# Optimization experiments

Measured on AMD Instinct MI355X. Metric: run time of the kernel, lower is better.

## Reference

```python
import jax, jax.numpy as jnp
import numpy as np

N = 100000
E = 600000
EL = 200000
HID = 16
HEADS = 4
NUM_NODE_TYPES = 8
NUM_EDGE_TYPES = 22
EDGE_DIM = 16


def setup_inputs() -> dict:
    key = jax.random.key(0)
    ks = jax.random.split(key, 32)
    s = 0.1
    d1, d2 = HID, HID * HEADS  # per-head dims of layer1 / layer2
    inp = {
        'x': jax.random.normal(ks[0], (N, HID), jnp.float32),
        'edge_index': jax.random.randint(ks[1], (2, E), 0, N),
        'node_type': jax.random.randint(ks[2], (N,), 0, NUM_NODE_TYPES),
        'edge_attr': jax.random.normal(ks[3], (E, EDGE_DIM), jnp.float32),
        'edge_type': jax.random.randint(ks[4], (E,), 0, NUM_EDGE_TYPES),
        'edge_label_index': jax.random.randint(ks[5], (2, EL), 0, N),
        # ---- layer 1 params (in=HID, heads=4, out-per-head=HID, concat) ----
        'Wx1': jax.random.normal(ks[6], (HID, HEADS * d1)) * s,
        'We1': jax.random.normal(ks[7], (EDGE_DIM, HEADS * d1)) * s,
        'nt1': jax.random.normal(ks[8], (NUM_NODE_TYPES, HID)) * s,
        'et1': jax.random.normal(ks[9], (NUM_EDGE_TYPES, HEADS * d1)) * s,
        'as1': jax.random.normal(ks[10], (HEADS, d1)) * s,
        'ad1': jax.random.normal(ks[11], (HEADS, d1)) * s,
        'ae1': jax.random.normal(ks[12], (HEADS, d1)) * s,
        'res1': jax.random.normal(ks[13], (HID, HEADS * d1)) * s,
        # ---- layer 2 params (in=4*HID, heads=4, out-per-head=4*HID, mean) ----
        'Wx2': jax.random.normal(ks[14], (HEADS * HID, HEADS * d2)) * s,
        'We2': jax.random.normal(ks[15], (EDGE_DIM, HEADS * d2)) * s,
        'nt2': jax.random.normal(ks[16], (NUM_NODE_TYPES, HEADS * HID)) * s,
        'et2': jax.random.normal(ks[17], (NUM_EDGE_TYPES, HEADS * d2)) * s,
        'as2': jax.random.normal(ks[18], (HEADS, d2)) * s,
        'ad2': jax.random.normal(ks[19], (HEADS, d2)) * s,
        'ae2': jax.random.normal(ks[20], (HEADS, d2)) * s,
        # ---- edge decoder (2*4*HID -> 4*HID -> 1) ----
        'W1': jax.random.normal(ks[21], (2 * HEADS * HID, HEADS * HID)) * s,
        'b1': jnp.zeros((HEADS * HID,), jnp.float32),
        'W2': jax.random.normal(ks[22], (HEADS * HID, 1)) * s,
        'b2': jnp.zeros((1,), jnp.float32),
    }
    return inp


def hgat_layer(x, edge_index, node_type, edge_attr, edge_type,
               Wx, We, nt_emb, et_emb, a_s, a_d, a_e, res_W,
               heads, d, concat, n):
    src, dst = edge_index[0], edge_index[1]
    # type-conditioned node projection -> [N, heads, d]
    h = ((x + nt_emb[node_type]) @ Wx).reshape(n, heads, d)
    # type-conditioned edge features -> [E, heads, d]
    e = (edge_attr @ We + et_emb[edge_type]).reshape(-1, heads, d)
    hs = h[src]  # [E, heads, d] gather
    hd = h[dst]
    sc = (jnp.einsum('ehd,hd->eh', hs, a_s)
          + jnp.einsum('ehd,hd->eh', hd, a_d)
          + jnp.einsum('ehd,hd->eh', e, a_e))
    sc = jax.nn.leaky_relu(sc, 0.2)
    # segment softmax over incoming edges of each destination node
    m = jax.ops.segment_max(sc, dst, num_segments=n)
    p = jnp.exp(sc - m[dst])
    den = jax.ops.segment_sum(p, dst, num_segments=n)
    alpha = p / (den[dst] + 1e-16)
    msg = alpha[:, :, None] * (hs + e)  # [E, heads, d]
    out = jax.ops.segment_sum(msg.reshape(-1, heads * d), dst, num_segments=n)
    out = out.reshape(n, heads, d)
    if concat:
        return out.reshape(n, heads * d) + x @ res_W
    else:
        return out.mean(axis=1) + x  # in-dim == out-dim: identity residual


def reference(x, edge_index, node_type, edge_attr, edge_type, edge_label_index,
              Wx1, We1, nt1, et1, as1, ad1, ae1, res1,
              Wx2, We2, nt2, et2, as2, ad2, ae2,
              W1, b1, W2, b2):
    n = x.shape[0]
    z = hgat_layer(x, edge_index, node_type, edge_attr, edge_type,
                   Wx1, We1, nt1, et1, as1, ad1, ae1, res1,
                   HEADS, HID, True, n)
    z = jax.nn.relu(z)
    z = hgat_layer(z, edge_index, node_type, edge_attr, edge_type,
                   Wx2, We2, nt2, et2, as2, ad2, ae2, None,
                   HEADS, HEADS * HID, False, n)
    # edge decoder: gather endpoint embeddings, 2-layer MLP
    row, col = edge_label_index[0], edge_label_index[1]
    zz = jnp.concatenate([z[row], z[col]], axis=-1)  # [EL, 2*4*HID]
    h = jax.nn.relu(zz @ W1 + b1)
    pred = (h @ W2 + b2).reshape(-1)
    return pred, z
```

## Files before the change

kernel.cpp:

```cpp
#include <hip/hip_runtime.h>
#include <stdint.h>

typedef unsigned short u16;
typedef unsigned int   u32;
typedef __attribute__((ext_vector_type(8))) short v8s;
typedef __attribute__((ext_vector_type(4))) float v4f;

#define NN  100000
#define NE  600000
#define NEL 200000

__device__ __forceinline__ float b2f(u16 u){ return __uint_as_float(((u32)u)<<16); }
__device__ __forceinline__ u16 f2b(float f){
  u32 u = __float_as_uint(f);
  u32 r = (u + 0x7FFFu + ((u>>16)&1u)) >> 16;
  return (u16)r;
}
__device__ __forceinline__ void unpack8(uint4 v, float* o){
  o[0]=__uint_as_float(v.x<<16); o[1]=__uint_as_float(v.x&0xffff0000u);
  o[2]=__uint_as_float(v.y<<16); o[3]=__uint_as_float(v.y&0xffff0000u);
  o[4]=__uint_as_float(v.z<<16); o[5]=__uint_as_float(v.z&0xffff0000u);
  o[6]=__uint_as_float(v.w<<16); o[7]=__uint_as_float(v.w&0xffff0000u);
}
__device__ __forceinline__ float ldf(const void* p, size_t i, int m){
  return m ? b2f(((const u16*)p)[i]) : ((const float*)p)[i];
}
__device__ __forceinline__ void ld16(const void* p, size_t off, int m, float* o){
  if (m){
    const uint4* q = (const uint4*)((const u16*)p + off);
    uint4 a=q[0], b=q[1]; unpack8(a,o); unpack8(b,o+8);
  } else {
    const float4* q = (const float4*)((const float*)p + off);
    float4 a=q[0],b=q[1],c=q[2],d=q[3];
    o[0]=a.x;o[1]=a.y;o[2]=a.z;o[3]=a.w; o[4]=b.x;o[5]=b.y;o[6]=b.z;o[7]=b.w;
    o[8]=c.x;o[9]=c.y;o[10]=c.z;o[11]=c.w; o[12]=d.x;o[13]=d.y;o[14]=d.z;o[15]=d.w;
  }
}
__device__ __forceinline__ void stf(void* p, size_t i, int m, float v){
  if (m) ((u16*)p)[i] = f2b(v); else ((float*)p)[i] = v;
}
__device__ __forceinline__ void atomAdd(float* p, float v){ unsafeAtomicAdd(p, v); }

__global__ void k_detect(const void* a0,const void* a3,const void* a6,const void* a7,
                         const void* a8,const void* a9,const void* a10,const void* a11,
                         const void* a12,const void* a13,const void* a14,const void* a15,
                         const void* a16,const void* a17,const void* a18,const void* a19,
                         const void* a20,const void* a21,const void* a23,
                         int* __restrict__ flags){
  const void* ptrs[19] = {a0,a3,a6,a7,a8,a9,a10,a11,a12,a13,a14,a15,a16,a17,a18,a19,a20,a21,a23};
  const int  idxs[19] = {0,3,6,7,8,9,10,11,12,13,14,15,16,17,18,19,20,21,23};
  int b = blockIdx.x;
  const u16* q = (const u16*)ptrs[b];
  u16 u = q[threadIdx.x];
  int e = (u>>7)&0xFF;
  bool good = (u==0) || (e>=110 && e<=141);
  unsigned long long m = __ballot(good);
  if (threadIdx.x==0) flags[idxs[b]] = (__popcll(m) >= 52) ? 1 : 0;
}

__global__ __launch_bounds__(256) void k_zero(float* __restrict__ buf, int n){
  int i = blockIdx.x*256 + threadIdx.x;
  if (i < n) buf[i] = 0.f;
}
__global__ __launch_bounds__(256) void k_stub(u16* __restrict__ out, int n){
  int i = blockIdx.x*256 + threadIdx.x;
  if (i < n) out[i] = 0;
}

__global__ __launch_bounds__(256) void k_pack(const void* __restrict__ Wx2,
                                              const int* __restrict__ flags,
                                              u32* __restrict__ Wxp){
  int m14 = flags[14];
  int i = blockIdx.x*256 + threadIdx.x;
  int k2=i>>8, col=i&255;
  u16 lo = f2b(ldf(Wx2,(size_t)(2*k2)*256+col,m14));
  u16 hi = f2b(ldf(Wx2,(size_t)(2*k2+1)*256+col,m14));
  Wxp[i] = ((u32)hi<<16)|lo;
}

__global__ __launch_bounds__(256) void k_hist(const int* __restrict__ ei, int* __restrict__ cnt){
  int e = blockIdx.x*256 + threadIdx.x;
  if (e < NE) atomicAdd(&cnt[ei[NE+e]], 1);
}
__global__ __launch_bounds__(256) void k_scan1(const int* __restrict__ cnt,
                                               int* __restrict__ row_ptr, int* __restrict__ bsum){
  __shared__ int sb[256];
  int i = blockIdx.x*256 + threadIdx.x, t = threadIdx.x;
  int c = (i < NN) ? cnt[i] : 0;
  sb[t] = c; __syncthreads();
  for (int off=1; off<256; off<<=1){
    int v = (t>=off) ? sb[t-off] : 0; __syncthreads();
    sb[t] += v; __syncthreads();
  }
  if (i < NN) row_ptr[i] = sb[t] - c;
  if (t == 255) bsum[blockIdx.x] = sb[255];
}
__global__ __launch_bounds__(512) void k_scan2(const int* __restrict__ bsum, int* __restrict__ boff){
  __shared__ int sb[512];
  int t = threadIdx.x;
  int nblk = (NN+255)/256;
  int c = (t < nblk) ? bsum[t] : 0;
  sb[t] = c; __syncthreads();
  for (int off=1; off<512; off<<=1){
    int v = (t>=off) ? sb[t-off] : 0; __syncthreads();
    sb[t] += v; __syncthreads();
  }
  boff[t] = sb[t] - c;
}
__global__ __launch_bounds__(256) void k_scan3(int* __restrict__ row_ptr, const int* __restrict__ boff){
  int i = blockIdx.x*256 + threadIdx.x;
  if (i < NN) row_ptr[i] += boff[blockIdx.x];
  if (i == 0) row_ptr[NN] = NE;
}
__global__ __launch_bounds__(256) void k_scatter(const int* __restrict__ ei, const int* __restrict__ etype,
                                                 const int* __restrict__ row_ptr,
                                                 int* __restrict__ cur, int* __restrict__ perm,
                                                 int* __restrict__ rank, int* __restrict__ se){
  int e = blockIdx.x*256 + threadIdx.x;
  if (e < NE){
    int d = ei[NE+e];
    int pos = row_ptr[d] + atomicAdd(&cur[d], 1);
    perm[pos] = e;
    rank[e] = pos;
    se[pos] = ei[e] | (etype[e]<<20);
  }
}

__global__ void k_fold(const void* __restrict__ We1, const void* __restrict__ ae1, const void* __restrict__ et1,
                       const void* __restrict__ We2, const void* __restrict__ ae2, const void* __restrict__ et2,
                       const int* __restrict__ flags,
                       float* We1a, float* et1a, float* We2a, float* et2a){
  int m7=flags[7], m12=flags[12], m9=flags[9], m15=flags[15], m20=flags[20], m17=flags[17];
  int t = threadIdx.x;
  if (t < 64){
    int k=t>>2, h=t&3; float s=0.f;
    for (int d=0; d<16; d++) s += ldf(We1,k*64+h*16+d,m7)*ldf(ae1,h*16+d,m12);
    We1a[t]=s;
  } else if (t < 152){
    int i=t-64; int k=i>>2, h=i&3; float s=0.f;
    for (int d=0; d<16; d++) s += ldf(et1,k*64+h*16+d,m9)*ldf(ae1,h*16+d,m12);
    et1a[i]=s;
  } else if (t < 216){
    int i=t-152; int k=i>>2, h=i&3; float s=0.f;
    for (int d=0; d<64; d++) s += ldf(We2,k*256+h*64+d,m15)*ldf(ae2,h*64+d,m20);
    We2a[i]=s;
  } else if (t < 304){
    int i=t-216; int k=i>>2, h=i&3; float s=0.f;
    for (int d=0; d<64; d++) s += ldf(et2,k*256+h*64+d,m17)*ldf(ae2,h*64+d,m20);
    et2a[i]=s;
  }
}

__global__ __launch_bounds__(256) void k1_node(
    const void* __restrict__ x, const int* __restrict__ ntype,
    const void* __restrict__ Wx1, const void* __restrict__ nt1, const void* __restrict__ res1,
    const void* __restrict__ as1, const void* __restrict__ ad1,
    const int* __restrict__ flags,
    float* __restrict__ h1, float* __restrict__ out1,
    float* __restrict__ ssrc1, float* __restrict__ sdst1){
  __shared__ float sWx[1024], sRes[1024], sA[64], sD[64], sNt[128];
  int m0=flags[0], m6=flags[6], m8=flags[8], m13=flags[13], m10=flags[10], m11=flags[11];
  for (int i=threadIdx.x;i<1024;i+=256){ sWx[i]=ldf(Wx1,i,m6); sRes[i]=ldf(res1,i,m13); }
  if (threadIdx.x<64){ sA[threadIdx.x]=ldf(as1,threadIdx.x,m10); sD[threadIdx.x]=ldf(ad1,threadIdx.x,m11); }
  if (threadIdx.x<128) sNt[threadIdx.x]=ldf(nt1,threadIdx.x,m8);
  __syncthreads();
  int n = blockIdx.x*256 + threadIdx.x;
  if (n >= NN) return;
  float xv[16]; ld16(x, (size_t)n*16, m0, xv);
  int nt = ntype[n];
  float xin[16];
  #pragma unroll
  for (int k=0;k<16;k++) xin[k] = xv[k] + sNt[nt*16+k];
  float ss[4]={0,0,0,0}, sd[4]={0,0,0,0};
  #pragma unroll
  for (int jq=0;jq<16;jq++){
    float sarr[4], rarr[4];
    #pragma unroll
    for (int m=0;m<4;m++){
      int j = jq*4+m;
      float s=0.f, r=0.f;
      #pragma unroll
      for (int k=0;k<16;k++){ s += xin[k]*sWx[k*64+j]; r += xv[k]*sRes[k*64+j]; }
      sarr[m]=s; rarr[m]=r;
      ss[j>>4] += s*sA[j];
      sd[j>>4] += s*sD[j];
    }
    ((float4*)(h1  + (size_t)n*64))[jq] = make_float4(sarr[0],sarr[1],sarr[2],sarr[3]);
    ((float4*)(out1+ (size_t)n*64))[jq] = make_float4(rarr[0],rarr[1],rarr[2],rarr[3]);
  }
  ((float4*)ssrc1)[n] = make_float4(ss[0],ss[1],ss[2],ss[3]);
  ((float4*)sdst1)[n] = make_float4(sd[0],sd[1],sd[2],sd[3]);
}

__global__ __launch_bounds__(256) void k_sed(
    const int* __restrict__ ei, const void* __restrict__ eattr, const int* __restrict__ etype,
    const float* __restrict__ Wea, const float* __restrict__ eta,
    const float* __restrict__ ssrc, const float* __restrict__ sdst,
    const int* __restrict__ rank,
    const int* __restrict__ flags,
    float* __restrict__ psort){
  __shared__ float sW[64], sE[88];
  int m3=flags[3];
  if (threadIdx.x<64) sW[threadIdx.x]=Wea[threadIdx.x];
  if (threadIdx.x<88) sE[threadIdx.x]=eta[threadIdx.x];
  __syncthreads();
  int e = blockIdx.x*256 + threadIdx.x;
  if (e >= NE) return;
  int s = ei[e], d = ei[NE+e], t = etype[e];
  float ea[16]; ld16(eattr, (size_t)e*16, m3, ea);
  float4 s4 = ((const float4*)ssrc)[s];
  float4 d4 = ((const float4*)sdst)[d];
  float sv[4] = { s4.x+d4.x, s4.y+d4.y, s4.z+d4.z, s4.w+d4.w };
  float pv[4];
  #pragma unroll
  for (int h=0; h<4; h++){
    float v = sE[t*4+h] + sv[h];
    #pragma unroll
    for (int k=0;k<16;k++) v += ea[k]*sW[k*4+h];
    v = v > 0.f ? v : 0.2f*v;
    v = fminf(v, 60.f);
    pv[h] = __expf(v);
  }
  ((float4*)psort)[rank[e]] = make_float4(pv[0],pv[1],pv[2],pv[3]);
}

__global__ __launch_bounds__(256) void k_msg1(
    const void* __restrict__ eattr, const void* __restrict__ et1, const void* __restrict__ We1,
    const float* __restrict__ h1, const float* __restrict__ psort,
    const int* __restrict__ row_ptr, const int* __restrict__ perm, const int* __restrict__ se,
    const int* __restrict__ flags,
    float* __restrict__ out1){
  __shared__ float sEt[22*64];
  __shared__ float sW1[16*64];
  __shared__ float sG[4][64];
  int m3=flags[3], m9=flags[9], m7=flags[7];
  for (int i=threadIdx.x;i<22*64;i+=256) sEt[i]=ldf(et1,i,m9);
  for (int i=threadIdx.x;i<16*64;i+=256) sW1[i]=ldf(We1,i,m7);
  __syncthreads();
  int j = threadIdx.x & 63;
  int h = j>>4, jk = j&15;
  int wid = threadIdx.x>>6;
  for (int it=0; it<8; ++it){
    int n = (blockIdx.x*4 + wid)*8 + it;
    int beg=row_ptr[n], end=row_ptr[n+1];
    float sp=0.f, acc=0.f, gacc=0.f;
    int i=beg;
    for (; i+1<end; i+=2){
      int st0=se[i], st1=se[i+1];
      float4 p0=((const float4*)psort)[i], p1=((const float4*)psort)[i+1];
      int pe0=perm[i], pe1=perm[i+1];
      int s0=st0&0xFFFFF, t0=st0>>20;
      int s1=st1&0xFFFFF, t1=st1>>20;
      float ph0 = (h==0?p0.x:h==1?p0.y:h==2?p0.z:p0.w);
      float ph1 = (h==0?p1.x:h==1?p1.y:h==2?p1.z:p1.w);
      float hv0 = h1[(size_t)s0*64+j];
      float hv1 = h1[(size_t)s1*64+j];
      float ea0 = ldf(eattr,(size_t)pe0*16+jk,m3);
      float ea1 = ldf(eattr,(size_t)pe1*16+jk,m3);
      sp   += ph0 + ph1;
      acc  += ph0*(hv0+sEt[t0*64+j]) + ph1*(hv1+sEt[t1*64+j]);
      gacc += ph0*ea0 + ph1*ea1;
    }
    if (i<end){
      int st0=se[i];
      float4 p0=((const float4*)psort)[i];
      int pe0=perm[i];
      int s0=st0&0xFFFFF, t0=st0>>20;
      float ph0 = (h==0?p0.x:h==1?p0.y:h==2?p0.z:p0.w);
      sp   += ph0;
      acc  += ph0*(h1[(size_t)s0*64+j]+sEt[t0*64+j]);
      gacc += ph0*ldf(eattr,(size_t)pe0*16+jk,m3);
    }
    float rd = 1.f/(sp+1e-16f);
    sG[wid][j] = gacc*rd;
    float proj=0.f;
    #pragma unroll
    for (int k=0;k<16;k++) proj += sG[wid][h*16+k]*sW1[k*64+j];
    out1[(size_t)n*64+j] += acc*rd + proj;
  }
}

__global__ __launch_bounds__(256) void k5_node2(
    const int* __restrict__ ntype,
    const u32* __restrict__ Wxp, const void* __restrict__ nt2,
    const void* __restrict__ as2, const void* __restrict__ ad2,
    const int* __restrict__ flags,
    const float* __restrict__ out1, float* __restrict__ zfin,
    u16* __restrict__ h2, float* __restrict__ ssrc2, float* __restrict__ sdst2){
  __shared__ u32   sWp[32*256];
  __shared__ float sNt[512];
  __shared__ float sAs[256], sAd[256];
  __shared__ float sZ[4][8][64];
  __shared__ float sR[4][2][256];
  int m16=flags[16], m18=flags[18], m19=flags[19];
  for (int i=threadIdx.x;i<32*256;i+=256) sWp[i] = Wxp[i];
  for (int i=threadIdx.x;i<512;i+=256) sNt[i]=ldf(nt2,i,m16);
  sAs[threadIdx.x]=ldf(as2,threadIdx.x,m18);
  sAd[threadIdx.x]=ldf(ad2,threadIdx.x,m19);
  __syncthreads();
  int slot=threadIdx.x>>6, j=threadIdx.x&63;
  int base=(blockIdx.x*4+slot)*8;
  #pragma unroll
  for (int i=0;i<8;i++){
    int n=base+i;
    float z = out1[(size_t)n*64+j]; z = fmaxf(z, 0.f);
    zfin[(size_t)n*64+j] = z;
    sZ[slot][i][j] = z + sNt[(ntype[n]<<6)|j];
  }
  __syncthreads();
  float acc[8][4];
  #pragma unroll
  for (int i=0;i<8;i++){ acc[i][0]=0;acc[i][1]=0;acc[i][2]=0;acc[i][3]=0; }
  for (int k2=0;k2<32;k2++){
    u32 w0p=sWp[k2*256+j], w1p=sWp[k2*256+64+j], w2p=sWp[k2*256+128+j], w3p=sWp[k2*256+192+j];
    float w0l=__uint_as_float(w0p<<16), w0h=__uint_as_float(w0p&0xffff0000u);
    float w1l=__uint_as_float(w1p<<16), w1h=__uint_as_float(w1p&0xffff0000u);
    float w2l=__uint_as_float(w2p<<16), w2h=__uint_as_float(w2p&0xffff0000u);
    float w3l=__uint_as_float(w3p<<16), w3h=__uint_as_float(w3p&0xffff0000u);
    #pragma unroll
    for (int i=0;i<8;i++){
      float2 zz = *(const float2*)&sZ[slot][i][k2*2];
      acc[i][0] += zz.x*w0l + zz.y*w0h;
      acc[i][1] += zz.x*w1l + zz.y*w1h;
      acc[i][2] += zz.x*w2l + zz.y*w2h;
      acc[i][3] += zz.x*w3l + zz.y*w3h;
    }
  }
  int g=j>>4, l=j&15;
  #pragma unroll
  for (int i=0;i<8;i++){
    int n=base+i;
    u32 lo = (u32)f2b(acc[i][0]) | ((u32)f2b(acc[i][1])<<16);
    u32 hi = (u32)f2b(acc[i][2]) | ((u32)f2b(acc[i][3])<<16);
    *(uint2*)&h2[(size_t)n*256 + j*4] = make_uint2(lo,hi);
    sR[slot][0][      j] = acc[i][0]*sAs[      j];
    sR[slot][0][ 64 + j] = acc[i][1]*sAs[ 64 + j];
    sR[slot][0][128 + j] = acc[i][2]*sAs[128 + j];
    sR[slot][0][192 + j] = acc[i][3]*sAs[192 + j];
    sR[slot][1][      j] = acc[i][0]*sAd[      j];
    sR[slot][1][ 64 + j] = acc[i][1]*sAd[ 64 + j];
    sR[slot][1][128 + j] = acc[i][2]*sAd[128 + j];
    sR[slot][1][192 + j] = acc[i][3]*sAd[192 + j];
    float4 v4 = *(const float4*)&sR[slot][0][g*64 + l*4];
    float4 w4 = *(const float4*)&sR[slot][1][g*64 + l*4];
    float vs = v4.x+v4.y+v4.z+v4.w;
    float vd = w4.x+w4.y+w4.z+w4.w;
    #pragma unroll
    for (int off=1; off<16; off<<=1){ vs += __shfl_xor(vs,off); vd += __shfl_xor(vd,off); }
    if (l==0){ ssrc2[(size_t)n*4+g]=vs; sdst2[(size_t)n*4+g]=vd; }
  }
}

__global__ __launch_bounds__(256) void k_msg2(
    const void* __restrict__ eattr, const void* __restrict__ et2,
    const u16* __restrict__ h2, const float* __restrict__ psort,
    const int* __restrict__ row_ptr, const int* __restrict__ perm, const int* __restrict__ se,
    const int* __restrict__ flags,
    float* __restrict__ zfin, float* __restrict__ gsum){
  __shared__ float4 sEt4[22*64];
  int m3=flags[3], m17=flags[17];
  for (int i=threadIdx.x;i<22*64;i+=256){
    int t=i>>6, j=i&63;
    sEt4[i] = make_float4(ldf(et2,(size_t)t*256+j,m17),      ldf(et2,(size_t)t*256+64+j,m17),
                          ldf(et2,(size_t)t*256+128+j,m17),  ldf(et2,(size_t)t*256+192+j,m17));
  }
  __syncthreads();
  int j = threadIdx.x & 63;
  int jh = j>>4, jk = j&15;
  int wid = threadIdx.x>>6;
  for (int it=0; it<8; ++it){
    int n = (blockIdx.x*4 + wid)*8 + it;
    int beg=row_ptr[n], end=row_ptr[n+1];
    float ds0=0,ds1=0,ds2=0,ds3=0;
    float pa0=0,pa1=0,pa2=0,pa3=0, gacc=0;
    int i=beg;
    for (; i+1<end; i+=2){
      int st0=se[i], st1=se[i+1];
      float4 q0=((const float4*)psort)[i], q1=((const float4*)psort)[i+1];
      int pe0=perm[i], pe1=perm[i+1];
      int s0=st0&0xFFFFF, t0=st0>>20;
      int s1=st1&0xFFFFF, t1=st1>>20;
      uint2 hA = *(const uint2*)&h2[(size_t)s0*256 + j*4];
      uint2 hB = *(const uint2*)&h2[(size_t)s1*256 + j*4];
      float ea0 = ldf(eattr,(size_t)pe0*16+jk,m3);
      float ea1 = ldf(eattr,(size_t)pe1*16+jk,m3);
      float4 eA = sEt4[t0*64+j], eB = sEt4[t1*64+j];
      ds0 += q0.x+q1.x; ds1 += q0.y+q1.y; ds2 += q0.z+q1.z; ds3 += q0.w+q1.w;
      pa0 += q0.x*(__uint_as_float(hA.x<<16)        +eA.x) + q1.x*(__uint_as_float(hB.x<<16)        +eB.x);
      pa1 += q0.y*(__uint_as_float(hA.x&0xffff0000u)+eA.y) + q1.y*(__uint_as_float(hB.x&0xffff0000u)+eB.y);
      pa2 += q0.z*(__uint_as_float(hA.y<<16)        +eA.z) + q1.z*(__uint_as_float(hB.y<<16)        +eB.z);
      pa3 += q0.w*(__uint_as_float(hA.y&0xffff0000u)+eA.w) + q1.w*(__uint_as_float(hB.y&0xffff0000u)+eB.w);
      float pj0 = (jh==0?q0.x:jh==1?q0.y:jh==2?q0.z:q0.w);
      float pj1 = (jh==0?q1.x:jh==1?q1.y:jh==2?q1.z:q1.w);
      gacc += pj0*ea0 + pj1*ea1;
    }
    if (i<end){
      int st0=se[i];
      float4 q0=((const float4*)psort)[i];
      int pe0=perm[i];
      int s0=st0&0xFFFFF, t0=st0>>20;
      uint2 hA = *(const uint2*)&h2[(size_t)s0*256 + j*4];
      float4 eA = sEt4[t0*64+j];
      ds0 += q0.x; ds1 += q0.y; ds2 += q0.z; ds3 += q0.w;
      pa0 += q0.x*(__uint_as_float(hA.x<<16)        +eA.x);
      pa1 += q0.y*(__uint_as_float(hA.x&0xffff0000u)+eA.y);
      pa2 += q0.z*(__uint_as_float(hA.y<<16)        +eA.z);
      pa3 += q0.w*(__uint_as_float(hA.y&0xffff0000u)+eA.w);
      float pj0 = (jh==0?q0.x:jh==1?q0.y:jh==2?q0.z:q0.w);
      gacc += pj0*ldf(eattr,(size_t)pe0*16+jk,m3);
    }
    float r0=1.f/(ds0+1e-16f), r1=1.f/(ds1+1e-16f), r2=1.f/(ds2+1e-16f), r3=1.f/(ds3+1e-16f);
    float acc = pa0*r0 + pa1*r1 + pa2*r2 + pa3*r3;
    float rj = (jh==0?r0:jh==1?r1:jh==2?r2:r3);
    zfin[(size_t)n*64+j] += 0.25f*acc;
    gsum[(size_t)n*64+j] = gacc*rj;
  }
}

__global__ __launch_bounds__(256) void k_finz(
    const float* __restrict__ gsum, const void* __restrict__ We2,
    const int* __restrict__ flags, float* __restrict__ zfin, void* __restrict__ out){
  __shared__ float sW[16*256];
  __shared__ float sG[4][64];
  int m15=flags[15], mo=flags[0];
  for (int i=threadIdx.x;i<16*256;i+=256) sW[i]=ldf(We2,i,m15);
  __syncthreads();
  int slot=threadIdx.x>>6, j=threadIdx.x&63;
  for (int nb=blockIdx.x; nb<NN/4; nb+=gridDim.x){
    int n = nb*4 + slot;
    sG[slot][j] = gsum[(size_t)n*64 + j];
    float acc = 0.f;
    #pragma unroll
    for (int h=0;h<4;h++){
      float s=0.f;
      #pragma unroll
      for (int k=0;k<16;k++) s += sG[slot][h*16+k]*sW[k*256 + h*64 + j];
      acc += s;
    }
    float zf = zfin[(size_t)n*64+j] + 0.25f*acc;
    zfin[(size_t)n*64+j] = zf;
    stf(out, (size_t)NEL + (size_t)n*64 + j, mo, zf);
  }
}

__global__ __launch_bounds__(256) void k_dec(
    const int* __restrict__ eli, const float* __restrict__ zfin,
    const void* __restrict__ W1, const u16* __restrict__ b1,
    const void* __restrict__ W2, const u16* __restrict__ b2,
    const int* __restrict__ flags,
    void* __restrict__ out){
  __shared__ v8s sB[4][4][64];
  __shared__ float sB1[64], sW2[64];
  int m21=flags[21], m23=flags[23], mo=flags[0];
  for (int idx=threadIdx.x; idx<1024; idx+=256){
    int kb=idx>>8, ct=(idx>>6)&3, l=idx&63;
    int col = ct*16 + (l&15);
    int kbase = kb*32 + ((l>>4)<<3);
    short v[8];
    #pragma unroll
    for (int i=0;i<8;i++) v[i] = (short)f2b(ldf(W1,(size_t)(kbase+i)*64+col,m21));
    sB[kb][ct][l] = *(v8s*)v;
  }
  if (threadIdx.x<64){ sB1[threadIdx.x]=b2f(b1[threadIdx.x]); sW2[threadIdx.x]=ldf(W2,threadIdx.x,m23); }
  __syncthreads();
  float b2v = b2f(b2[0]);
  int w = threadIdx.x>>6, lane = threadIdx.x&63;
  int l15 = lane&15, lk = lane>>4;
  int ngrp = NEL/64;
  for (int g = blockIdx.x; g < ngrp; g += gridDim.x){
    int e0 = g*64 + w*16;
    int eA = e0 + l15;
    int rn = eli[eA], cn = eli[NEL+eA];
    v8s a[4];
    #pragma unroll
    for (int kb=0;kb<4;kb++){
      int k = kb*32 + lk*8;
      const float* src = (k<64) ? (zfin + (size_t)rn*64 + k) : (zfin + (size_t)cn*64 + (k-64));
      float4 f0 = *(const float4*)(src);
      float4 f1 = *(const float4*)(src+4);
      short v[8] = {(short)f2b(f0.x),(short)f2b(f0.y),(short)f2b(f0.z),(short)f2b(f0.w),
                    (short)f2b(f1.x),(short)f2b(f1.y),(short)f2b(f1.z),(short)f2b(f1.w)};
      a[kb] = *(v8s*)v;
    }
    float part[4] = {0,0,0,0};
    #pragma unroll
    for (int ct=0; ct<4; ct++){
      v4f c = {0.f,0.f,0.f,0.f};
      #pragma unroll
      for (int kb=0;kb<4;kb++)
        c = __builtin_amdgcn_mfma_f32_16x16x32_bf16(a[kb], sB[kb][ct][lane], c, 0,0,0);
      int col = ct*16 + l15;
      float w2c = sW2[col], b1c = sB1[col];
      #pragma unroll
      for (int r=0;r<4;r++) part[r] += fmaxf(c[r]+b1c, 0.f) * w2c;
    }
    #pragma unroll
    for (int r=0;r<4;r++){
      float v = part[r];
      #pragma unroll
      for (int off=1; off<16; off<<=1) v += __shfl_xor(v, off);
      if (l15==0) stf(out, e0 + lk*4 + r, mo, v + b2v);
    }
  }
}

extern "C" void kernel_launch(void* const* d_in, const int* in_sizes, int n_in,
                              void* d_out, int out_size, void* d_ws, size_t ws_size,
                              hipStream_t stream){
  (void)in_sizes; (void)n_in;
  const void* x    =d_in[0];
  const int* ei    =(const int*)d_in[1];
  const int* ntype =(const int*)d_in[2];
  const void* eattr=d_in[3];
  const int* etype =(const int*)d_in[4];
  const int* eli   =(const int*)d_in[5];
  const void* Wx1=d_in[6];  const void* We1=d_in[7];  const void* nt1=d_in[8];
  const void* et1=d_in[9];  const void* as1=d_in[10]; const void* ad1=d_in[11];
  const void* ae1=d_in[12]; const void* res1=d_in[13];
  const void* Wx2=d_in[14]; const void* We2=d_in[15]; const void* nt2=d_in[16];
  const void* et2=d_in[17]; const void* as2=d_in[18]; const void* ad2=d_in[19];
  const void* ae2=d_in[20];
  const void* W1=d_in[21];  const u16* b1=(const u16*)d_in[22];
  const void* W2=d_in[23];  const u16* b2=(const u16*)d_in[24];

  const size_t NEED_BYTES = 30809572ULL * 4ULL;
  if (ws_size < NEED_BYTES){
    k_stub<<<(out_size+255)/256,256,0,stream>>>((u16*)d_out, out_size);
    return;
  }
  float* ws=(float*)d_ws;
  size_t o=0;
  int*   flags=(int*)(ws+o); o+=32;
  float* We1a =ws+o; o+=64;
  float* et1a =ws+o; o+=96;
  float* We2a =ws+o; o+=64;
  float* et2a =ws+o; o+=96;
  int*   cnt    =(int*)(ws+o); o+=NN;
  int*   row_ptr=(int*)(ws+o); o+=NN+4;
  int*   perm   =(int*)(ws+o); o+=NE;
  int*   bsum   =(int*)(ws+o); o+=512;
  int*   boff   =(int*)(ws+o); o+=512;
  int*   rank   =(int*)(ws+o); o+=NE;
  int*   se     =(int*)(ws+o); o+=NE;
  u32*   Wxp    =(u32*)(ws+o); o+=8192;
  float* ssrc =ws+o; o+=(size_t)NN*4;
  float* sdst =ws+o; o+=(size_t)NN*4;
  float* psort=ws+o; o+=(size_t)NE*4;
  float* slotA=ws+o; o+=(size_t)NN*64;
  float* out1 =ws+o; o+=(size_t)NN*64;
  u16*   h2   =(u16*)(ws+o); o+=(size_t)NN*128;
  float* h1   = slotA;
  float* zfin = slotA;
  float* gsum = out1;

  const int NBLK = (NN+255)/256;

  k_detect<<<19,64,0,stream>>>(x,eattr,Wx1,We1,nt1,et1,as1,ad1,ae1,res1,
                               Wx2,We2,nt2,et2,as2,ad2,ae2,W1,W2,flags);
  k_fold<<<1,320,0,stream>>>(We1,ae1,et1,We2,ae2,et2,flags,We1a,et1a,We2a,et2a);
  k_pack<<<32,256,0,stream>>>(Wx2,flags,Wxp);
  k_zero<<<(NN+255)/256,256,0,stream>>>((float*)cnt, NN);
  k_hist<<<(NE+255)/256,256,0,stream>>>(ei, cnt);
  k_scan1<<<NBLK,256,0,stream>>>(cnt, row_ptr, bsum);
  k_scan2<<<1,512,0,stream>>>(bsum, boff);
  k_scan3<<<NBLK,256,0,stream>>>(row_ptr, boff);
  k_zero<<<(NN+255)/256,256,0,stream>>>((float*)cnt, NN);
  k_scatter<<<(NE+255)/256,256,0,stream>>>(ei, etype, row_ptr, cnt, perm, rank, se);
  k1_node<<<(NN+255)/256,256,0,stream>>>(x,ntype,Wx1,nt1,res1,as1,ad1,flags,h1,out1,ssrc,sdst);
  k_sed<<<(NE+255)/256,256,0,stream>>>(ei,eattr,etype,We1a,et1a,ssrc,sdst,rank,flags,psort);
  k_msg1<<<NN/32,256,0,stream>>>(eattr,et1,We1,h1,psort,row_ptr,perm,se,flags,out1);
  k5_node2<<<NN/32,256,0,stream>>>(ntype,Wxp,nt2,as2,ad2,flags,out1,zfin,h2,ssrc,sdst);
  k_sed<<<(NE+255)/256,256,0,stream>>>(ei,eattr,etype,We2a,et2a,ssrc,sdst,rank,flags,psort);
  k_msg2<<<NN/32,256,0,stream>>>(eattr,et2,h2,psort,row_ptr,perm,se,flags,zfin,gsum);
  k_finz<<<2048,256,0,stream>>>(gsum,We2,flags,zfin,d_out);
  k_dec<<<1024,256,0,stream>>>(eli,zfin,W1,b1,W2,b2,flags,d_out);
}
```

Measured before the change: 618.9 us.

## Fuse edge attention score computation into message aggregation kernels

Removes the separate k_sed kernels that computed per-edge exp-scores into a sorted psort buffer, and drops the rank array. Each message kernel now recomputes the score inline from the edge attributes it already loads, using a 16-lane shuffle reduction against the folded edge weights plus gathered ssrc/sdst values. This saves two full edge passes, including the scattered psort writes and the later psort reads. In exchange the inner loop gains shuffles, exp and extra ssrc gathers, and layer 2 needs cross-head broadcasts.

```diff
diff --git a/kernel.cpp b/kernel.cpp
--- a/kernel.cpp
+++ b/kernel.cpp
@@ -115,13 +115,12 @@
 __global__ __launch_bounds__(256) void k_scatter(const int* __restrict__ ei, const int* __restrict__ etype,
                                                  const int* __restrict__ row_ptr,
                                                  int* __restrict__ cur, int* __restrict__ perm,
-                                                 int* __restrict__ rank, int* __restrict__ se){
+                                                 int* __restrict__ se){
   int e = blockIdx.x*256 + threadIdx.x;
   if (e < NE){
     int d = ei[NE+e];
     int pos = row_ptr[d] + atomicAdd(&cur[d], 1);
     perm[pos] = e;
-    rank[e] = pos;
     se[pos] = ei[e] | (etype[e]<<20);
   }
 }
@@ -192,84 +191,72 @@
   ((float4*)sdst1)[n] = make_float4(sd[0],sd[1],sd[2],sd[3]);
 }
 
-__global__ __launch_bounds__(256) void k_sed(
-    const int* __restrict__ ei, const void* __restrict__ eattr, const int* __restrict__ etype,
-    const float* __restrict__ Wea, const float* __restrict__ eta,
-    const float* __restrict__ ssrc, const float* __restrict__ sdst,
-    const int* __restrict__ rank,
-    const int* __restrict__ flags,
-    float* __restrict__ psort){
-  __shared__ float sW[64], sE[88];
-  int m3=flags[3];
-  if (threadIdx.x<64) sW[threadIdx.x]=Wea[threadIdx.x];
-  if (threadIdx.x<88) sE[threadIdx.x]=eta[threadIdx.x];
-  __syncthreads();
-  int e = blockIdx.x*256 + threadIdx.x;
-  if (e >= NE) return;
-  int s = ei[e], d = ei[NE+e], t = etype[e];
-  float ea[16]; ld16(eattr, (size_t)e*16, m3, ea);
-  float4 s4 = ((const float4*)ssrc)[s];
-  float4 d4 = ((const float4*)sdst)[d];
-  float sv[4] = { s4.x+d4.x, s4.y+d4.y, s4.z+d4.z, s4.w+d4.w };
-  float pv[4];
-  #pragma unroll
-  for (int h=0; h<4; h++){
-    float v = sE[t*4+h] + sv[h];
-    #pragma unroll
-    for (int k=0;k<16;k++) v += ea[k]*sW[k*4+h];
-    v = v > 0.f ? v : 0.2f*v;
-    v = fminf(v, 60.f);
-    pv[h] = __expf(v);
-  }
-  ((float4*)psort)[rank[e]] = make_float4(pv[0],pv[1],pv[2],pv[3]);
-}
-
 __global__ __launch_bounds__(256) void k_msg1(
     const void* __restrict__ eattr, const void* __restrict__ et1, const void* __restrict__ We1,
-    const float* __restrict__ h1, const float* __restrict__ psort,
+    const float* __restrict__ We1a, const float* __restrict__ et1a,
+    const float* __restrict__ ssrc, const float* __restrict__ sdst,
+    const float* __restrict__ h1,
     const int* __restrict__ row_ptr, const int* __restrict__ perm, const int* __restrict__ se,
     const int* __restrict__ flags,
     float* __restrict__ out1){
   __shared__ float sEt[22*64];
   __shared__ float sW1[16*64];
+  __shared__ float sWa[64], sEa[88];
   __shared__ float sG[4][64];
   int m3=flags[3], m9=flags[9], m7=flags[7];
   for (int i=threadIdx.x;i<22*64;i+=256) sEt[i]=ldf(et1,i,m9);
   for (int i=threadIdx.x;i<16*64;i+=256) sW1[i]=ldf(We1,i,m7);
+  if (threadIdx.x<64) sWa[threadIdx.x]=We1a[threadIdx.x];
+  if (threadIdx.x<88) sEa[threadIdx.x]=et1a[threadIdx.x];
   __syncthreads();
   int j = threadIdx.x & 63;
   int h = j>>4, jk = j&15;
   int wid = threadIdx.x>>6;
+  float wA = sWa[jk*4+h];
   for (int it=0; it<8; ++it){
     int n = (blockIdx.x*4 + wid)*8 + it;
+    float sdn = sdst[(size_t)n*4+h];
     int beg=row_ptr[n], end=row_ptr[n+1];
     float sp=0.f, acc=0.f, gacc=0.f;
     int i=beg;
     for (; i+1<end; i+=2){
       int st0=se[i], st1=se[i+1];
-      float4 p0=((const float4*)psort)[i], p1=((const float4*)psort)[i+1];
       int pe0=perm[i], pe1=perm[i+1];
       int s0=st0&0xFFFFF, t0=st0>>20;
       int s1=st1&0xFFFFF, t1=st1>>20;
-      float ph0 = (h==0?p0.x:h==1?p0.y:h==2?p0.z:p0.w);
-      float ph1 = (h==0?p1.x:h==1?p1.y:h==2?p1.z:p1.w);
+      float ea0 = ldf(eattr,(size_t)pe0*16+jk,m3);
+      float ea1 = ldf(eattr,(size_t)pe1*16+jk,m3);
       float hv0 = h1[(size_t)s0*64+j];
       float hv1 = h1[(size_t)s1*64+j];
+      float ss0 = ssrc[(size_t)s0*4+h];
+      float ss1 = ssrc[(size_t)s1*4+h];
+      float sc0 = ea0*wA, sc1 = ea1*wA;
+      sc0 += __shfl_xor(sc0,1); sc1 += __shfl_xor(sc1,1);
+      sc0 += __shfl_xor(sc0,2); sc1 += __shfl_xor(sc1,2);
+      sc0 += __shfl_xor(sc0,4); sc1 += __shfl_xor(sc1,4);
+      sc0 += __shfl_xor(sc0,8); sc1 += __shfl_xor(sc1,8);
+      float v0 = sEa[t0*4+h] + ss0 + sdn + sc0;
+      float v1 = sEa[t1*4+h] + ss1 + sdn + sc1;
+      v0 = v0>0.f ? v0 : 0.2f*v0;  v0 = fminf(v0,60.f);  float p0 = __expf(v0);
+      v1 = v1>0.f ? v1 : 0.2f*v1;  v1 = fminf(v1,60.f);  float p1 = __expf(v1);
+      sp   += p0 + p1;
+      acc  += p0*(hv0+sEt[t0*64+j]) + p1*(hv1+sEt[t1*64+j]);
+      gacc += p0*ea0 + p1*ea1;
+    }
+    if (i<end){
+      int st0=se[i]; int pe0=perm[i];
+      int s0=st0&0xFFFFF, t0=st0>>20;
       float ea0 = ldf(eattr,(size_t)pe0*16+jk,m3);
-      float ea1 = ldf(eattr,(size_t)pe1*16+jk,m3);
-      sp   += ph0 + ph1;
-      acc  += ph0*(hv0+sEt[t0*64+j]) + ph1*(hv1+sEt[t1*64+j]);
-      gacc += ph0*ea0 + ph1*ea1;
-    }
-    if (i<end){
-      int st0=se[i];
-      float4 p0=((const float4*)psort)[i];
-      int pe0=perm[i];
-      int s0=st0&0xFFFFF, t0=st0>>20;
-      float ph0 = (h==0?p0.x:h==1?p0.y:h==2?p0.z:p0.w);
-      sp   += ph0;
-      acc  += ph0*(h1[(size_t)s0*64+j]+sEt[t0*64+j]);
-      gacc += ph0*ldf(eattr,(size_t)pe0*16+jk,m3);
+      float hv0 = h1[(size_t)s0*64+j];
+      float ss0 = ssrc[(size_t)s0*4+h];
+      float sc0 = ea0*wA;
+      sc0 += __shfl_xor(sc0,1); sc0 += __shfl_xor(sc0,2);
+      sc0 += __shfl_xor(sc0,4); sc0 += __shfl_xor(sc0,8);
+      float v0 = sEa[t0*4+h] + ss0 + sdn + sc0;
+      v0 = v0>0.f ? v0 : 0.2f*v0;  v0 = fminf(v0,60.f);  float p0 = __expf(v0);
+      sp   += p0;
+      acc  += p0*(hv0+sEt[t0*64+j]);
+      gacc += p0*ea0;
     }
     float rd = 1.f/(sp+1e-16f);
     sG[wid][j] = gacc*rd;
@@ -353,61 +340,83 @@
 
 __global__ __launch_bounds__(256) void k_msg2(
     const void* __restrict__ eattr, const void* __restrict__ et2,
-    const u16* __restrict__ h2, const float* __restrict__ psort,
+    const float* __restrict__ We2a, const float* __restrict__ et2a,
+    const float* __restrict__ ssrc, const float* __restrict__ sdst,
+    const u16* __restrict__ h2,
     const int* __restrict__ row_ptr, const int* __restrict__ perm, const int* __restrict__ se,
     const int* __restrict__ flags,
     float* __restrict__ zfin, float* __restrict__ gsum){
   __shared__ float4 sEt4[22*64];
+  __shared__ float sWa[64], sEa[88];
   int m3=flags[3], m17=flags[17];
   for (int i=threadIdx.x;i<22*64;i+=256){
     int t=i>>6, j=i&63;
     sEt4[i] = make_float4(ldf(et2,(size_t)t*256+j,m17),      ldf(et2,(size_t)t*256+64+j,m17),
                           ldf(et2,(size_t)t*256+128+j,m17),  ldf(et2,(size_t)t*256+192+j,m17));
   }
+  if (threadIdx.x<64) sWa[threadIdx.x]=We2a[threadIdx.x];
+  if (threadIdx.x<88) sEa[threadIdx.x]=et2a[threadIdx.x];
   __syncthreads();
   int j = threadIdx.x & 63;
   int jh = j>>4, jk = j&15;
   int wid = threadIdx.x>>6;
+  float wA = sWa[jk*4+jh];
   for (int it=0; it<8; ++it){
     int n = (blockIdx.x*4 + wid)*8 + it;
+    float sdn = sdst[(size_t)n*4+jh];
     int beg=row_ptr[n], end=row_ptr[n+1];
     float ds0=0,ds1=0,ds2=0,ds3=0;
     float pa0=0,pa1=0,pa2=0,pa3=0, gacc=0;
     int i=beg;
     for (; i+1<end; i+=2){
       int st0=se[i], st1=se[i+1];
-      float4 q0=((const float4*)psort)[i], q1=((const float4*)psort)[i+1];
       int pe0=perm[i], pe1=perm[i+1];
       int s0=st0&0xFFFFF, t0=st0>>20;
       int s1=st1&0xFFFFF, t1=st1>>20;
+      float ea0 = ldf(eattr,(size_t)pe0*16+jk,m3);
+      float ea1 = ldf(eattr,(size_t)pe1*16+jk,m3);
       uint2 hA = *(const uint2*)&h2[(size_t)s0*256 + j*4];
       uint2 hB = *(const uint2*)&h2[(size_t)s1*256 + j*4];
+      float ss0 = ssrc[(size_t)s0*4+jh];
+      float ss1 = ssrc[(size_t)s1*4+jh];
+      float sc0 = ea0*wA, sc1 = ea1*wA;
+      sc0 += __shfl_xor(sc0,1); sc1 += __shfl_xor(sc1,1);
+      sc0 += __shfl_xor(sc0,2); sc1 += __shfl_xor(sc1,2);
+      sc0 += __shfl_xor(sc0,4); sc1 += __shfl_xor(sc1,4);
+      sc0 += __shfl_xor(sc0,8); sc1 += __shfl_xor(sc1,8);
+      float v0 = sEa[t0*4+jh] + ss0 + sdn + sc0;
+      float v1 = sEa[t1*4+jh] + ss1 + sdn + sc1;
+      v0 = v0>0.f ? v0 : 0.2f*v0;  v0 = fminf(v0,60.f);  float p0 = __expf(v0);
+      v1 = v1>0.f ? v1 : 0.2f*v1;  v1 = fminf(v1,60.f);  float p1 = __expf(v1);
+      float q0x=__shfl(p0,0), q0y=__shfl(p0,16), q0z=__shfl(p0,32), q0w=__shfl(p0,48);
+      float q1x=__shfl(p1,0), q1y=__shfl(p1,16), q1z=__shfl(p1,32), q1w=__shfl(p1,48);
+      float4 eA = sEt4[t0*64+j], eB = sEt4[t1*64+j];
+      ds0 += q0x+q1x; ds1 += q0y+q1y; ds2 += q0z+q1z; ds3 += q0w+q1w;
+      pa0 += q0x*(__uint_as_float(hA.x<<16)        +eA.x) + q1x*(__uint_as_float(hB.x<<16)        +eB.x);
+      pa1 += q0y*(__uint_as_float(hA.x&0xffff0000u)+eA.y) + q1y*(__uint_as_float(hB.x&0xffff0000u)+eB.y);
+      pa2 += q0z*(__uint_as_float(hA.y<<16)        +eA.z) + q1z*(__uint_as_float(hB.y<<16)        +eB.z);
+      pa3 += q0w*(__uint_as_float(hA.y&0xffff0000u)+eA.w) + q1w*(__uint_as_float(hB.y&0xffff0000u)+eB.w);
+      gacc += p0*ea0 + p1*ea1;
+    }
+    if (i<end){
+      int st0=se[i]; int pe0=perm[i];
+      int s0=st0&0xFFFFF, t0=st0>>20;
       float ea0 = ldf(eattr,(size_t)pe0*16+jk,m3);
-      float ea1 = ldf(eattr,(size_t)pe1*16+jk,m3);
-      float4 eA = sEt4[t0*64+j], eB = sEt4[t1*64+j];
-      ds0 += q0.x+q1.x; ds1 += q0.y+q1.y; ds2 += q0.z+q1.z; ds3 += q0.w+q1.w;
-      pa0 += q0.x*(__uint_as_float(hA.x<<16)        +eA.x) + q1.x*(__uint_as_float(hB.x<<16)        +eB.x);
-      pa1 += q0.y*(__uint_as_float(hA.x&0xffff0000u)+eA.y) + q1.y*(__uint_as_float(hB.x&0xffff0000u)+eB.y);
-      pa2 += q0.z*(__uint_as_float(hA.y<<16)        +eA.z) + q1.z*(__uint_as_float(hB.y<<16)        +eB.z);
-      pa3 += q0.w*(__uint_as_float(hA.y&0xffff0000u)+eA.w) + q1.w*(__uint_as_float(hB.y&0xffff0000u)+eB.w);
-      float pj0 = (jh==0?q0.x:jh==1?q0.y:jh==2?q0.z:q0.w);
-      float pj1 = (jh==0?q1.x:jh==1?q1.y:jh==2?q1.z:q1.w);
-      gacc += pj0*ea0 + pj1*ea1;
-    }
-    if (i<end){
-      int st0=se[i];
-      float4 q0=((const float4*)psort)[i];
-      int pe0=perm[i];
-      int s0=st0&0xFFFFF, t0=st0>>20;
       uint2 hA = *(const uint2*)&h2[(size_t)s0*256 + j*4];
+      float ss0 = ssrc[(size_t)s0*4+jh];
+      float sc0 = ea0*wA;
+      sc0 += __shfl_xor(sc0,1); sc0 += __shfl_xor(sc0,2);
+      sc0 += __shfl_xor(sc0,4); sc0 += __shfl_xor(sc0,8);
+      float v0 = sEa[t0*4+jh] + ss0 + sdn + sc0;
+      v0 = v0>0.f ? v0 : 0.2f*v0;  v0 = fminf(v0,60.f);  float p0 = __expf(v0);
+      float q0x=__shfl(p0,0), q0y=__shfl(p0,16), q0z=__shfl(p0,32), q0w=__shfl(p0,48);
       float4 eA = sEt4[t0*64+j];
-      ds0 += q0.x; ds1 += q0.y; ds2 += q0.z; ds3 += q0.w;
-      pa0 += q0.x*(__uint_as_float(hA.x<<16)        +eA.x);
-      pa1 += q0.y*(__uint_as_float(hA.x&0xffff0000u)+eA.y);
-      pa2 += q0.z*(__uint_as_float(hA.y<<16)        +eA.z);
-      pa3 += q0.w*(__uint_as_float(hA.y&0xffff0000u)+eA.w);
-      float pj0 = (jh==0?q0.x:jh==1?q0.y:jh==2?q0.z:q0.w);
-      gacc += pj0*ldf(eattr,(size_t)pe0*16+jk,m3);
+      ds0 += q0x; ds1 += q0y; ds2 += q0z; ds3 += q0w;
+      pa0 += q0x*(__uint_as_float(hA.x<<16)        +eA.x);
+      pa1 += q0y*(__uint_as_float(hA.x&0xffff0000u)+eA.y);
+      pa2 += q0z*(__uint_as_float(hA.y<<16)        +eA.z);
+      pa3 += q0w*(__uint_as_float(hA.y&0xffff0000u)+eA.w);
+      gacc += p0*ea0;
     }
     float r0=1.f/(ds0+1e-16f), r1=1.f/(ds1+1e-16f), r2=1.f/(ds2+1e-16f), r3=1.f/(ds3+1e-16f);
     float acc = pa0*r0 + pa1*r1 + pa2*r2 + pa3*r3;
@@ -549,6 +558,7 @@
   float* slotA=ws+o; o+=(size_t)NN*64;
   float* out1 =ws+o; o+=(size_t)NN*64;
   u16*   h2   =(u16*)(ws+o); o+=(size_t)NN*128;
+  (void)rank; (void)psort;
   float* h1   = slotA;
   float* zfin = slotA;
   float* gsum = out1;
@@ -565,13 +575,11 @@
   k_scan2<<<1,512,0,stream>>>(bsum, boff);
   k_scan3<<<NBLK,256,0,stream>>>(row_ptr, boff);
   k_zero<<<(NN+255)/256,256,0,stream>>>((float*)cnt, NN);
-  k_scatter<<<(NE+255)/256,256,0,stream>>>(ei, etype, row_ptr, cnt, perm, rank, se);
+  k_scatter<<<(NE+255)/256,256,0,stream>>>(ei, etype, row_ptr, cnt, perm, se);
   k1_node<<<(NN+255)/256,256,0,stream>>>(x,ntype,Wx1,nt1,res1,as1,ad1,flags,h1,out1,ssrc,sdst);
-  k_sed<<<(NE+255)/256,256,0,stream>>>(ei,eattr,etype,We1a,et1a,ssrc,sdst,rank,flags,psort);
-  k_msg1<<<NN/32,256,0,stream>>>(eattr,et1,We1,h1,psort,row_ptr,perm,se,flags,out1);
+  k_msg1<<<NN/32,256,0,stream>>>(eattr,et1,We1,We1a,et1a,ssrc,sdst,h1,row_ptr,perm,se,flags,out1);
   k5_node2<<<NN/32,256,0,stream>>>(ntype,Wxp,nt2,as2,ad2,flags,out1,zfin,h2,ssrc,sdst);
-  k_sed<<<(NE+255)/256,256,0,stream>>>(ei,eattr,etype,We2a,et2a,ssrc,sdst,rank,flags,psort);
-  k_msg2<<<NN/32,256,0,stream>>>(eattr,et2,h2,psort,row_ptr,perm,se,flags,zfin,gsum);
+  k_msg2<<<NN/32,256,0,stream>>>(eattr,et2,We2a,et2a,ssrc,sdst,h2,row_ptr,perm,se,flags,zfin,gsum);
   k_finz<<<2048,256,0,stream>>>(gsum,We2,flags,zfin,d_out);
   k_dec<<<1024,256,0,stream>>>(eli,zfin,W1,b1,W2,b2,flags,d_out);
 }
```

Result: slower. 642.0 us (+3.7%).
